# Kernel tuning notes

Hardware: AMD Instinct MI355X
Metric: run time of the kernel (lower is better)

## Reference

```python
import jax, jax.numpy as jnp
from jax import lax
import numpy as np

WAY = 100
SHOT = 5
QUERY = 15
D = 4096
LAM = 10.0
ALPHA = 0.2
N_EPOCHS = 20
EPS = 1e-6
MAXITERS = 1000
N_L = WAY * SHOT          # 500 labeled
N_U = WAY * QUERY         # 1500 unlabeled
N_TOT = N_L + N_U         # 2000


def setup_inputs() -> dict:
    key = jax.random.key(0)
    kx, = jax.random.split(key, 1)
    X = jax.random.uniform(kx, (N_TOT, D), dtype=jnp.float32)  # features must be >= 0
    # data is ordered as (shot+query) blocks of `way` samples, one per class
    labels = jnp.tile(jnp.arange(WAY, dtype=jnp.int32), SHOT + QUERY)
    return {"X": X, "labels": labels}


def _normalize(X):
    # F.normalize(p=2, dim=-1) with eps=1e-12
    return X / jnp.maximum(jnp.linalg.norm(X, axis=-1, keepdims=True), 1e-12)


def _cdist(X, Y):
    # Euclidean distances [n, m] via gram trick (avoids [n, m, d] intermediate)
    d2 = (X * X).sum(-1)[:, None] + (Y * Y).sum(-1)[None, :] - 2.0 * (X @ Y.T)
    return jnp.sqrt(jnp.maximum(d2, 1e-12))


def _sinkhorn(M, r, c):
    # Row/col scaling loop of compute_optimal_transport, tracked via scaling
    # vectors (a, b) so P_k = a * K * b exactly matches the in-place updates.
    K = jnp.exp(-LAM * M)
    K = K / K.sum()
    n, m = M.shape

    def step(carry, _):
        a, b, prev, done = carry
        rowsum = a * (K @ b)                       # P.sum(-1)
        err = jnp.max(jnp.abs(prev - rowsum))      # convergence check vs old u
        done = done | (err <= EPS)
        a_new = jnp.where(done, a, a * r / rowsum)
        colsum = b * (K.T @ a_new)                 # P.sum(1) after row scaling
        b_new = jnp.where(done, b, b * c / colsum)
        prev_new = jnp.where(done, prev, rowsum)
        return (a_new, b_new, prev_new, done), None

    init = (jnp.ones(n, M.dtype), jnp.ones(m, M.dtype),
            jnp.zeros(n, M.dtype), jnp.array(False))
    (a, b, _, _), _ = lax.scan(step, init, None, length=MAXITERS)
    return a[:, None] * K * b[None, :]


def _forward(X, labels):
    # power transform
    X = jnp.sqrt(X + 1e-6)
    # scale (mode='val'): normalize -> center labeled/unlabeled separately -> normalize
    X = _normalize(X)
    Xl = X[:N_L] - X[:N_L].mean(0, keepdims=True)
    Xu = X[N_L:] - X[N_L:].mean(0, keepdims=True)
    Z = _normalize(jnp.concatenate([Xl, Xu], axis=0))

    # init class means from labeled shots
    mus0 = Z.reshape(SHOT + QUERY, WAY, -1)[:SHOT].mean(0)  # [way, d]

    r = jnp.ones(N_U, Z.dtype)
    c = jnp.full((WAY,), float(QUERY), Z.dtype)
    onehot = jax.nn.one_hot(labels[:N_L], WAY, dtype=Z.dtype)

    def get_probas(mus):
        dist = _cdist(Z, mus)                      # [n_tot, way]
        Pu = _sinkhorn(dist[N_L:], r, c)           # [n_u, way]
        return jnp.concatenate([onehot, Pu], axis=0)

    def epoch(mus, _):
        p = get_probas(mus)
        emus = (p.T @ Z) / p.sum(0)[:, None]       # estimate_from_mask
        return mus + ALPHA * (emus - mus), None    # update_from_estimate

    mus, _ = lax.scan(epoch, mus0, None, length=N_EPOCHS)

    P = get_probas(mus)
    logP = jnp.log(P[N_L:] + 1e-5)
    acc = (jnp.argmax(P[N_L:], axis=-1) == labels[N_L:]).astype(jnp.float32).mean()
    return logP, acc


def reference(X, labels):
    return _forward(X, labels)
```

## Files before the change

### kernel.cpp

```cpp
#include <hip/hip_runtime.h>

#define WAY   100
#define SHOT  5
#define NQ    15
#define DD    4096
#define N_L   500
#define N_U   1500
#define N_TOT 2000
#define LAMF  10.0f
#define EPSF  1e-6f
#define MAXIT 1000

#define OFF_Z      0u
#define OFF_CPP    3145728u
#define OFF_MEANL  8192000u
#define OFF_MEANU  8196096u
#define OFF_SL     8200192u
#define OFF_MUSA   8609792u
#define OFF_MUSB   9068544u
#define OFF_MUSQP  9527296u
#define OFF_MUSB16 9552896u
#define OFF_PTH    9782272u
#define OFF_PTL    9868288u
#define OFF_KMAT   9954304u
#define OFF_COLS   10104320u
#define OFF_MISC   10113920u
#define OFF_ZUT    10114688u
#define OFF_ZUTL   13260416u
#define OFF_AG     16406144u
#define OFF_PREVG  16407680u
#define OFF_BINIT  16409216u

#define SINK_BLOCKS 32
#define RPB 47
#define PTS 1536
#define CPS 409600u

typedef __attribute__((ext_vector_type(8))) short short8_t;
typedef __attribute__((ext_vector_type(4))) float f32x4;

__device__ __forceinline__ short f2bs(float f) {
  unsigned u = __float_as_uint(f);
  unsigned r = (u + 0x7FFFu + ((u >> 16) & 1u)) >> 16;
  return (short)r;
}
__device__ __forceinline__ float bs2f(short s) {
  return __uint_as_float(((unsigned)(unsigned short)s) << 16);
}

__global__ __launch_bounds__(256) void k_pow_norm(const float* __restrict__ X, float* __restrict__ Z,
                                                  float* __restrict__ msums, unsigned* __restrict__ misc_u,
                                                  float* __restrict__ aG) {
  int i = blockIdx.x, tid = threadIdx.x;
  __shared__ float red[256];
  if (i < 32) msums[i * 256 + tid] = 0.f;
  if (i == 32) { misc_u[tid] = 0u; misc_u[tid + 256] = 0u; misc_u[tid + 512] = 0u; }
  if (i == 33) { for (int z = tid; z < 1504; z += 256) aG[z] = -1.f; }
  const float* x = X + (size_t)i * DD;
  float s = 0.f;
  for (int k = tid; k < DD; k += 256) s += x[k] + 1e-6f;
  red[tid] = s; __syncthreads();
  for (int o = 128; o > 0; o >>= 1) { if (tid < o) red[tid] += red[tid + o]; __syncthreads(); }
  float inv = 1.0f / fmaxf(sqrtf(red[0]), 1e-12f);
  float* z = Z + (size_t)i * DD;
  for (int k = tid; k < DD; k += 256) z[k] = sqrtf(x[k] + 1e-6f) * inv;
}

__global__ __launch_bounds__(256) void k_colmeans(const float* __restrict__ Z, float* __restrict__ mLs,
                                                  float* __restrict__ mUs) {
  int k = blockIdx.x * 256 + threadIdx.x;
  int r0 = blockIdx.y * 80;
  float sL = 0.f, sU = 0.f;
  for (int r = r0; r < r0 + 80; ++r) {
    float v = Z[(size_t)r * DD + k];
    if (r < N_L) sL += v; else sU += v;
  }
  if (r0 < N_L) atomicAdd(&mLs[k], sL);
  if (r0 + 80 > N_L) atomicAdd(&mUs[k], sU);
}

__global__ __launch_bounds__(256) void k_center(float* __restrict__ Z, const float* __restrict__ mLs,
                                                const float* __restrict__ mUs) {
  int i = blockIdx.x, tid = threadIdx.x;
  __shared__ float red[256];
  const float* m = (i < N_L) ? mLs : mUs;
  const float scale = (i < N_L) ? (1.0f / 500.0f) : (1.0f / 1500.0f);
  float* z = Z + (size_t)i * DD;
  float s = 0.f;
  for (int k = tid; k < DD; k += 256) { float v = z[k] - m[k] * scale; s += v * v; }
  red[tid] = s; __syncthreads();
  for (int o = 128; o > 0; o >>= 1) { if (tid < o) red[tid] += red[tid + o]; __syncthreads(); }
  float inv = 1.0f / fmaxf(sqrtf(red[0]), 1e-12f);
  for (int k = tid; k < DD; k += 256) z[k] = (z[k] - m[k] * scale) * inv;
}

__global__ __launch_bounds__(256) void k_musinit(const float* __restrict__ Z, float* __restrict__ SL,
                                                 float* __restrict__ mus, short* __restrict__ musb,
                                                 float* __restrict__ musqP, float* __restrict__ binit) {
  int w = blockIdx.x, tid = threadIdx.x;
  __shared__ float red[256];
  if (tid == 0) binit[w] = 1.0f;
  float q = 0.f;
  for (int k = tid; k < DD; k += 256) {
    float s = 0.f;
    for (int sh = 0; sh < SHOT; ++sh) s += Z[(size_t)(sh * WAY + w) * DD + k];
    SL[(size_t)w * DD + k] = s;
    float m = s / 5.0f;
    mus[(size_t)w * DD + k] = m;
    musb[(size_t)w * DD + k] = f2bs(m);
    q += m * m;
  }
  red[tid] = q; __syncthreads();
  for (int o = 128; o > 0; o >>= 1) { if (tid < o) red[tid] += red[tid + o]; __syncthreads(); }
  if (tid == 0) musqP[(size_t)w * 256] = red[0];
  else musqP[(size_t)w * 256 + tid] = 0.f;
}

__global__ __launch_bounds__(256) void k_zb(const float* __restrict__ Z, short* __restrict__ Zb, int ubase) {
  size_t i0 = (size_t)ubase * DD + ((size_t)blockIdx.x * 256 + threadIdx.x) * 8;
  short8_t v;
  if (i0 < (size_t)N_U * DD) {
    const float* src = Z + (size_t)N_L * DD + i0;
    float4 a = *(const float4*)src;
    float4 b = *(const float4*)(src + 4);
    v[0] = f2bs(a.x); v[1] = f2bs(a.y); v[2] = f2bs(a.z); v[3] = f2bs(a.w);
    v[4] = f2bs(b.x); v[5] = f2bs(b.y); v[6] = f2bs(b.z); v[7] = f2bs(b.w);
  } else {
    v = (short8_t){0, 0, 0, 0, 0, 0, 0, 0};
  }
  *(short8_t*)(Zb + i0) = v;
}

__global__ __launch_bounds__(256) void k_zt(const float* __restrict__ Z, short* __restrict__ ZTH,
                                            short* __restrict__ ZTL) {
  __shared__ float tile[32][33];
  int k0 = blockIdx.x * 32, u0 = blockIdx.y * 32;
  int c = threadIdx.x & 31, r0 = threadIdx.x >> 5;
#pragma unroll
  for (int rr = 0; rr < 4; ++rr) {
    int r = r0 + rr * 8;
    int u = u0 + r;
    tile[r][c] = (u < N_U) ? Z[(size_t)(N_L + u) * DD + k0 + c] : 0.f;
  }
  __syncthreads();
#pragma unroll
  for (int rr = 0; rr < 4; ++rr) {
    int r = r0 + rr * 8;
    float v = tile[c][r];
    short hi = f2bs(v);
    ZTH[(size_t)(k0 + r) * PTS + u0 + c] = hi;
    ZTL[(size_t)(k0 + r) * PTS + u0 + c] = f2bs(v - bs2f(hi));
  }
}

__global__ __launch_bounds__(256) void k_gemm1K(const short* __restrict__ Zb, const short* __restrict__ musb,
                                                const float* __restrict__ musqP, float* __restrict__ Kmat,
                                                unsigned* __restrict__ misc_u) {
  int tid = threadIdx.x;
  __shared__ float redA[4 * 7 * 4 * 64];
  __shared__ float musq2[2][128];
  if (blockIdx.x == 0) {
    for (int z = tid; z < 768; z += 256) misc_u[z] = 0u;
  }
  {
    int w = tid >> 1, half = tid & 1;
    if (w < WAY) {
      const float* mp = musqP + (size_t)w * 256 + half * 128;
      float q = 0.f;
#pragma unroll 4
      for (int bb = 0; bb < 128; bb += 4) {
        float4 v4 = *(const float4*)(mp + bb);
        q += (v4.x + v4.y) + (v4.z + v4.w);
      }
      musq2[half][w] = q;
    }
  }
  int wv = tid >> 6, l = tid & 63;
  int l15 = l & 15, quad = (l >> 4) & 3;
  int u0 = blockIdx.x * 16;
  f32x4 acc[7];
#pragma unroll
  for (int c = 0; c < 7; ++c) acc[c] = (f32x4){0.f, 0.f, 0.f, 0.f};

  const short* bp = Zb + (size_t)(u0 + l15) * DD + wv * 1024 + quad * 8;
  const short* ap = musb + (size_t)l15 * DD + wv * 1024 + quad * 8;
#pragma unroll 2
  for (int kc = 0; kc < 1024; kc += 32) {
    short8_t bf = *(const short8_t*)(bp + kc);
#pragma unroll
    for (int c = 0; c < 7; ++c) {
      short8_t af = *(const short8_t*)(ap + (size_t)c * 16 * DD + kc);
      acc[c] = __builtin_amdgcn_mfma_f32_16x16x32_bf16(af, bf, acc[c], 0, 0, 0);
    }
  }
#pragma unroll
  for (int c = 0; c < 7; ++c)
#pragma unroll
    for (int r = 0; r < 4; ++r)
      redA[((wv * 7 + c) * 4 + r) * 64 + l] = acc[c][r];
  __syncthreads();
  if (wv == 0) {
    int u = u0 + l15;
#pragma unroll
    for (int c = 0; c < 7; ++c)
#pragma unroll
      for (int r = 0; r < 4; ++r) {
        int base = (c * 4 + r) * 64 + l;
        float s = redA[base] + redA[base + 1792] + redA[base + 3584] + redA[base + 5376];
        int w = 16 * c + quad * 4 + r;
        if (w < WAY && u < N_U) {
          float d2 = 1.0f + (musq2[0][w] + musq2[1][w]) - 2.0f * s;
          Kmat[(size_t)u * WAY + w] = expf(-LAMF * sqrtf(fmaxf(d2, 1e-12f)));
        }
      }
  }
}

__device__ __forceinline__ void gbar(unsigned* slots, unsigned t) {
  __syncthreads();
  if (threadIdx.x == 0) {
    __threadfence();
    __hip_atomic_store(slots + (unsigned)blockIdx.x * 16, t, __ATOMIC_RELEASE, __HIP_MEMORY_SCOPE_AGENT);
  }
  if (threadIdx.x < SINK_BLOCKS) {
    while (__hip_atomic_load(slots + threadIdx.x * 16, __ATOMIC_ACQUIRE, __HIP_MEMORY_SCOPE_AGENT) < t)
      __builtin_amdgcn_s_sleep(1);
  }
  __syncthreads();
}

__global__ __launch_bounds__(256) void k_sink(const float* __restrict__ Kg,
                                              short* __restrict__ PTH, short* __restrict__ PTL,
                                              float* __restrict__ colsP, float* __restrict__ aG,
                                              float* __restrict__ prevG, float* __restrict__ binit,
                                              unsigned* __restrict__ misc_u, float* __restrict__ misc_f) {
  __shared__ float Kl[RPB * WAY];
  __shared__ float a[RPB], aold[RPB], prevs[RPB], b[WAY];
  __shared__ float rerr[256];
  __shared__ float c2[2 * WAY];
  __shared__ float red[256];
  __shared__ float eSh;
  unsigned* slots = misc_u + 8;
  float* KsumG = misc_f + 3;
  int tid = threadIdx.x;
  int row0 = blockIdx.x * RPB;
  int nrows = (row0 + RPB <= N_U) ? RPB : (N_U - row0);

  float ks = 0.f;
  for (int idx = tid; idx < nrows * WAY; idx += 256) { float v = Kg[row0 * WAY + idx]; Kl[idx] = v; ks += v; }
  red[tid] = ks; __syncthreads();
  for (int o = 128; o > 0; o >>= 1) { if (tid < o) red[tid] += red[tid + o]; __syncthreads(); }
  if (tid == 0) atomicAdd(KsumG, red[0]);
  if (tid < WAY) b[tid] = binit[tid];
  unsigned bt = 1;
  gbar(slots, bt);
  float S = *KsumG;
  bool warm = (aG[row0] >= 0.f);
  if (tid < RPB) {
    a[tid] = warm ? aG[row0 + tid] : (1.0f / S);
    prevs[tid] = warm ? prevG[row0 + tid] : 0.f;
  }

  bool conv = false;
  for (int t = 0; t < MAXIT; ++t) {
    float* cp = colsP + (t & 1) * 4096;
    __syncthreads();
    if (tid < nrows) {
      const float* kr = &Kl[tid * WAY];
      float r0 = 0.f, r1 = 0.f, r2 = 0.f, r3 = 0.f;
#pragma unroll 4
      for (int j = 0; j < WAY; j += 4) {
        r0 = fmaf(kr[j], b[j], r0);
        r1 = fmaf(kr[j + 1], b[j + 1], r1);
        r2 = fmaf(kr[j + 2], b[j + 2], r2);
        r3 = fmaf(kr[j + 3], b[j + 3], r3);
      }
      float rs = ((r0 + r1) + (r2 + r3)) * a[tid];
      rerr[tid] = fabsf(prevs[tid] - rs);
      aold[tid] = a[tid];
      a[tid] = a[tid] / rs;
      prevs[tid] = rs;
    } else {
      rerr[tid] = 0.f;
    }
    __syncthreads();
    {
      int j = -1, rlo = 0, rhi = 0, slot = 0;
      if (tid < WAY) { j = tid; rlo = 0; rhi = 24; slot = 0; }
      else if (tid >= 128 && tid < 128 + WAY) { j = tid - 128; rlo = 24; rhi = RPB; slot = 1; }
      if (j >= 0) {
        if (rhi > nrows) rhi = nrows;
        float pc = 0.f;
        for (int r = rlo; r < rhi; ++r) pc = fmaf(Kl[r * WAY + j], a[r], pc);
        c2[slot * WAY + j] = pc;
      }
    }
    __syncthreads();
    if (tid < WAY) cp[(unsigned)blockIdx.x * 128 + tid] = c2[tid] + c2[WAY + tid];
    if (tid < 64) {
      float m = fmaxf(fmaxf(rerr[tid], rerr[tid + 64]), fmaxf(rerr[tid + 128], rerr[tid + 192]));
#pragma unroll
      for (int o = 32; o > 0; o >>= 1) m = fmaxf(m, __shfl_down(m, o));
      if (tid == 0) cp[(unsigned)blockIdx.x * 128 + 100] = m;
    }
    ++bt;
    gbar(slots, bt);
    if (tid < 64) {
      float e = (tid < SINK_BLOCKS) ? cp[tid * 128 + 100] : 0.f;
#pragma unroll
      for (int o = 32; o > 0; o >>= 1) e = fmaxf(e, __shfl_down(e, o));
      if (tid == 0) eSh = e;
    }
    __syncthreads();
    if (eSh <= EPSF) { conv = true; break; }
    if (tid < WAY) {
      float s = 0.f;
#pragma unroll 8
      for (int sb = 0; sb < SINK_BLOCKS; ++sb) s += cp[sb * 128 + tid];
      b[tid] = (float)NQ / s;
    }
  }
  __syncthreads();
  if (tid < nrows) {
    float af = conv ? aold[tid] : a[tid];
    aG[row0 + tid] = af;
    prevG[row0 + tid] = prevs[tid];
  }
  if (blockIdx.x == 0 && tid < WAY) binit[tid] = b[tid];
  for (int idx = tid; idx < WAY * nrows; idx += 256) {
    int j = idx / nrows; int r = idx - j * nrows;
    float av = conv ? aold[r] : a[r];
    float p = av * Kl[r * WAY + j] * b[j];
    short hi = f2bs(p);
    PTH[(size_t)j * PTS + row0 + r] = hi;
    PTL[(size_t)j * PTS + row0 + r] = f2bs(p - bs2f(hi));
  }
  if (blockIdx.x == SINK_BLOCKS - 1) {
    for (int idx = tid; idx < WAY * 4; idx += 256) {
      int j = idx >> 2;
      PTH[(size_t)j * PTS + 1500 + (idx & 3)] = 0;
      PTL[(size_t)j * PTS + 1500 + (idx & 3)] = 0;
    }
  }
}

__global__ __launch_bounds__(64) void k_gemm2(const short* __restrict__ PTH, const short* __restrict__ PTL,
                                              const short* __restrict__ ZTH, const short* __restrict__ ZTL,
                                              float* __restrict__ CPp) {
  int l = threadIdx.x, l15 = l & 15, quad = l >> 4;
  int k0 = blockIdx.x * 16;
  int us = blockIdx.y;
  int kcb = us * 192;
  int kce = (us == 7) ? 1504 : kcb + 192;
  f32x4 acc[7];
#pragma unroll
  for (int c = 0; c < 7; ++c) acc[c] = (f32x4){0.f, 0.f, 0.f, 0.f};
  size_t aoff = (size_t)l15 * PTS + quad * 8;
  const short* bph = ZTH + (size_t)(k0 + l15) * PTS + quad * 8;
  const short* bpl = ZTL + (size_t)(k0 + l15) * PTS + quad * 8;
  for (int kc = kcb; kc < kce; kc += 32) {
    short8_t bh = *(const short8_t*)(bph + kc);
    short8_t bl = *(const short8_t*)(bpl + kc);
#pragma unroll
    for (int c = 0; c < 7; ++c) {
      short8_t ah = *(const short8_t*)(PTH + aoff + (size_t)c * 16 * PTS + kc);
      short8_t al = *(const short8_t*)(PTL + aoff + (size_t)c * 16 * PTS + kc);
      acc[c] = __builtin_amdgcn_mfma_f32_16x16x32_bf16(ah, bh, acc[c], 0, 0, 0);
      acc[c] = __builtin_amdgcn_mfma_f32_16x16x32_bf16(al, bh, acc[c], 0, 0, 0);
      acc[c] = __builtin_amdgcn_mfma_f32_16x16x32_bf16(ah, bl, acc[c], 0, 0, 0);
    }
  }
  float* dst = CPp + (size_t)us * CPS;
#pragma unroll
  for (int c = 0; c < 7; ++c)
#pragma unroll
    for (int r = 0; r < 4; ++r) {
      int w = 16 * c + quad * 4 + r;
      if (w < WAY) dst[(size_t)w * DD + k0 + l15] = acc[c][r];
    }
}

__global__ __launch_bounds__(256) void k_musup(const float* __restrict__ musR, const float* __restrict__ SL,
                                               const float* __restrict__ CPp, float* __restrict__ musW,
                                               short* __restrict__ musb, float* __restrict__ musqP) {
  int w = blockIdx.x, tid = threadIdx.x;
  int kb = blockIdx.y * 1024;
  __shared__ float red[256];
  float q = 0.f;
  for (int k = kb + tid; k < kb + 1024; k += 256) {
    size_t o = (size_t)w * DD + k;
    float c = 0.f;
#pragma unroll
    for (int s = 0; s < 8; ++s) c += CPp[(size_t)s * CPS + o];
    float emus = (SL[o] + c) / 20.0f;
    float m = musR[o];
    float v = m + 0.2f * (emus - m);
    musW[o] = v;
    musb[o] = f2bs(v);
    q += v * v;
  }
  red[tid] = q; __syncthreads();
  for (int o = 128; o > 0; o >>= 1) { if (tid < o) red[tid] += red[tid + o]; __syncthreads(); }
  if (tid == 0) musqP[(size_t)w * 256 + blockIdx.y] = red[0];
}

__global__ __launch_bounds__(128) void k_final(const short* __restrict__ PTH, const short* __restrict__ PTL,
                                               const int* __restrict__ labels, float* __restrict__ out,
                                               unsigned* __restrict__ ctr) {
  int u = blockIdx.x, tid = threadIdx.x;
  __shared__ float vals[WAY];
  if (tid < WAY) {
    float v = bs2f(PTH[(size_t)tid * PTS + u]) + bs2f(PTL[(size_t)tid * PTS + u]);
    vals[tid] = v;
    out[(size_t)u * WAY + tid] = logf(v + 1e-5f);
  }
  __syncthreads();
  if (tid == 0) {
    int am = 0; float bv = vals[0];
    for (int j = 1; j < WAY; ++j) { if (vals[j] > bv) { bv = vals[j]; am = j; } }
    if (am == labels[N_L + u]) atomicAdd(ctr, 1u);
  }
}

__global__ void k_acc(const unsigned* __restrict__ ctr, float* __restrict__ out) {
  if (threadIdx.x == 0) out[N_U * WAY] = (float)(*ctr) / 1500.0f;
}

extern "C" void kernel_launch(void* const* d_in, const int* in_sizes, int n_in,
                              void* d_out, int out_size, void* d_ws, size_t ws_size,
                              hipStream_t stream) {
  const float* X = (const float*)d_in[0];
  const int* labels = (const int*)d_in[1];
  float* out = (float*)d_out;
  float* ws = (float*)d_ws;

  float* Z     = ws + OFF_Z;
  short* Zb    = (short*)(ws + OFF_Z);
  float* CPp   = ws + OFF_CPP;
  float* meanL = ws + OFF_MEANL;
  float* meanU = ws + OFF_MEANU;
  float* SL    = ws + OFF_SL;
  float* musA  = ws + OFF_MUSA;
  float* musB  = ws + OFF_MUSB;
  float* musqP = ws + OFF_MUSQP;
  short* musb16 = (short*)(ws + OFF_MUSB16);
  short* PTH   = (short*)(ws + OFF_PTH);
  short* PTL   = (short*)(ws + OFF_PTL);
  float* Kmat  = ws + OFF_KMAT;
  float* colsP = ws + OFF_COLS;
  float* misc_f = ws + OFF_MISC;
  unsigned* misc_u = (unsigned*)(ws + OFF_MISC);
  short* ZTH   = (short*)(ws + OFF_ZUT);
  short* ZTL   = (short*)(ws + OFF_ZUTL);
  float* aG    = ws + OFF_AG;
  float* prevG = ws + OFF_PREVG;
  float* binit = ws + OFF_BINIT;

  k_pow_norm<<<N_TOT, 256, 0, stream>>>(X, Z, meanL, misc_u, aG);
  k_colmeans<<<dim3(16, 25), 256, 0, stream>>>(Z, meanL, meanU);
  k_center<<<N_TOT, 256, 0, stream>>>(Z, meanL, meanU);
  k_musinit<<<WAY, 256, 0, stream>>>(Z, SL, musA, musb16, musqP, binit);
  k_zt<<<dim3(128, 48), 256, 0, stream>>>(Z, ZTH, ZTL);
  k_zb<<<1536, 256, 0, stream>>>(Z, Zb, 0);
  k_zb<<<1536, 256, 0, stream>>>(Z, Zb, 768);

  float* musR = musA;
  float* musW = musB;
  for (int e = 0; e < 20; ++e) {
    k_gemm1K<<<96, 256, 0, stream>>>(Zb, musb16, musqP, Kmat, misc_u);
    k_sink<<<SINK_BLOCKS, 256, 0, stream>>>(Kmat, PTH, PTL, colsP, aG, prevG, binit, misc_u, misc_f);
    k_gemm2<<<dim3(256, 8), 64, 0, stream>>>(PTH, PTL, ZTH, ZTL, CPp);
    k_musup<<<dim3(WAY, 4), 256, 0, stream>>>(musR, SL, CPp, musW, musb16, musqP);
    float* tmp = musR; musR = musW; musW = tmp;
  }
  k_gemm1K<<<96, 256, 0, stream>>>(Zb, musb16, musqP, Kmat, misc_u);
  k_sink<<<SINK_BLOCKS, 256, 0, stream>>>(Kmat, PTH, PTL, colsP, aG, prevG, binit, misc_u, misc_f);
  k_final<<<N_U, 128, 0, stream>>>(PTH, PTL, labels, out, misc_u + 5);
  k_acc<<<1, 64, 0, stream>>>(misc_u + 5, out);
}
```

Baseline: 2.274 ms.

## Shrink Sinkhorn grid to 8 wide blocks and lighten grid barrier

The persistent Sinkhorn kernel now runs on 8 blocks of 512 threads with 188 rows each, instead of 32 blocks of 256. This cuts the number of participants in the per-iteration grid barrier and the size of the cross-block column reduction. The barrier drops release/acquire fences in favour of an explicit s_waitcnt plus relaxed agent-scope atomics, and the initial barrier is skipped on warm-started epochs. Shared K rows are padded to 101 floats to avoid bank conflicts, and the b update is computed before the convergence sync. In exchange, each block does more serial per-iteration work, and the memory ordering is weaker than before.

```diff
diff --git a/kernel.cpp b/kernel.cpp
--- a/kernel.cpp
+++ b/kernel.cpp
@@ -31,8 +31,10 @@
 #define OFF_PREVG  16407680u
 #define OFF_BINIT  16409216u
 
-#define SINK_BLOCKS 32
-#define RPB 47
+#define SINK_BLOCKS 8
+#define SINK_T 512
+#define RPB 188
+#define KLS 101
 #define PTS 1536
 #define CPS 409600u
 
@@ -46,6 +48,13 @@
 }
 __device__ __forceinline__ float bs2f(short s) {
   return __uint_as_float(((unsigned)(unsigned short)s) << 16);
+}
+
+__device__ __forceinline__ float ld_agent(const float* p) {
+  return __hip_atomic_load(p, __ATOMIC_RELAXED, __HIP_MEMORY_SCOPE_AGENT);
+}
+__device__ __forceinline__ void st_agent(float* p, float v) {
+  __hip_atomic_store(p, v, __ATOMIC_RELAXED, __HIP_MEMORY_SCOPE_AGENT);
 }
 
 __global__ __launch_bounds__(256) void k_pow_norm(const float* __restrict__ X, float* __restrict__ Z,
@@ -219,26 +228,26 @@
 __device__ __forceinline__ void gbar(unsigned* slots, unsigned t) {
   __syncthreads();
   if (threadIdx.x == 0) {
-    __threadfence();
-    __hip_atomic_store(slots + (unsigned)blockIdx.x * 16, t, __ATOMIC_RELEASE, __HIP_MEMORY_SCOPE_AGENT);
+    asm volatile("s_waitcnt vmcnt(0) lgkmcnt(0)" ::: "memory");
+    __hip_atomic_store(slots + (unsigned)blockIdx.x * 16, t, __ATOMIC_RELAXED, __HIP_MEMORY_SCOPE_AGENT);
   }
   if (threadIdx.x < SINK_BLOCKS) {
-    while (__hip_atomic_load(slots + threadIdx.x * 16, __ATOMIC_ACQUIRE, __HIP_MEMORY_SCOPE_AGENT) < t)
+    while (__hip_atomic_load(slots + threadIdx.x * 16, __ATOMIC_RELAXED, __HIP_MEMORY_SCOPE_AGENT) < t)
       __builtin_amdgcn_s_sleep(1);
   }
   __syncthreads();
 }
 
-__global__ __launch_bounds__(256) void k_sink(const float* __restrict__ Kg,
-                                              short* __restrict__ PTH, short* __restrict__ PTL,
-                                              float* __restrict__ colsP, float* __restrict__ aG,
-                                              float* __restrict__ prevG, float* __restrict__ binit,
-                                              unsigned* __restrict__ misc_u, float* __restrict__ misc_f) {
-  __shared__ float Kl[RPB * WAY];
+__global__ __launch_bounds__(SINK_T) void k_sink(const float* __restrict__ Kg,
+                                                 short* __restrict__ PTH, short* __restrict__ PTL,
+                                                 float* __restrict__ colsP, float* __restrict__ aG,
+                                                 float* __restrict__ prevG, float* __restrict__ binit,
+                                                 unsigned* __restrict__ misc_u, float* __restrict__ misc_f) {
+  __shared__ float Kl[RPB * KLS];
   __shared__ float a[RPB], aold[RPB], prevs[RPB], b[WAY];
-  __shared__ float rerr[256];
-  __shared__ float c2[2 * WAY];
-  __shared__ float red[256];
+  __shared__ float rerr[SINK_T];
+  __shared__ float c2[5 * WAY];
+  __shared__ float red[SINK_T];
   __shared__ float eSh;
   unsigned* slots = misc_u + 8;
   float* KsumG = misc_f + 3;
@@ -247,15 +256,21 @@
   int nrows = (row0 + RPB <= N_U) ? RPB : (N_U - row0);
 
   float ks = 0.f;
-  for (int idx = tid; idx < nrows * WAY; idx += 256) { float v = Kg[row0 * WAY + idx]; Kl[idx] = v; ks += v; }
+  for (int idx = tid; idx < nrows * WAY; idx += SINK_T) {
+    float v = Kg[row0 * WAY + idx];
+    int r = idx / WAY, j = idx - r * WAY;
+    Kl[r * KLS + j] = v;
+    ks += v;
+  }
   red[tid] = ks; __syncthreads();
-  for (int o = 128; o > 0; o >>= 1) { if (tid < o) red[tid] += red[tid + o]; __syncthreads(); }
+  for (int o = SINK_T / 2; o > 0; o >>= 1) { if (tid < o) red[tid] += red[tid + o]; __syncthreads(); }
   if (tid == 0) atomicAdd(KsumG, red[0]);
   if (tid < WAY) b[tid] = binit[tid];
-  unsigned bt = 1;
-  gbar(slots, bt);
-  float S = *KsumG;
+
   bool warm = (aG[row0] >= 0.f);
+  unsigned bt = 0;
+  if (!warm) { ++bt; gbar(slots, bt); }
+  float S = warm ? 1.f : ld_agent(KsumG);
   if (tid < RPB) {
     a[tid] = warm ? aG[row0 + tid] : (1.0f / S);
     prevs[tid] = warm ? prevG[row0 + tid] : 0.f;
@@ -266,7 +281,7 @@
     float* cp = colsP + (t & 1) * 4096;
     __syncthreads();
     if (tid < nrows) {
-      const float* kr = &Kl[tid * WAY];
+      const float* kr = &Kl[tid * KLS];
       float r0 = 0.f, r1 = 0.f, r2 = 0.f, r3 = 0.f;
 #pragma unroll 4
       for (int j = 0; j < WAY; j += 4) {
@@ -284,41 +299,47 @@
       rerr[tid] = 0.f;
     }
     __syncthreads();
-    {
-      int j = -1, rlo = 0, rhi = 0, slot = 0;
-      if (tid < WAY) { j = tid; rlo = 0; rhi = 24; slot = 0; }
-      else if (tid >= 128 && tid < 128 + WAY) { j = tid - 128; rlo = 24; rhi = RPB; slot = 1; }
-      if (j >= 0) {
-        if (rhi > nrows) rhi = nrows;
-        float pc = 0.f;
-        for (int r = rlo; r < rhi; ++r) pc = fmaf(Kl[r * WAY + j], a[r], pc);
-        c2[slot * WAY + j] = pc;
-      }
+    if (tid < 500) {
+      int slot = tid / 100;
+      int j = tid - slot * 100;
+      int rlo = slot * 38;
+      int rhi = rlo + 38; if (rhi > nrows) rhi = nrows;
+      float pc = 0.f;
+      for (int r = rlo; r < rhi; ++r) pc = fmaf(Kl[r * KLS + j], a[r], pc);
+      c2[slot * WAY + j] = pc;
     }
     __syncthreads();
-    if (tid < WAY) cp[(unsigned)blockIdx.x * 128 + tid] = c2[tid] + c2[WAY + tid];
+    if (tid < WAY) {
+      float s0 = c2[tid] + c2[WAY + tid] + c2[2 * WAY + tid] + c2[3 * WAY + tid] + c2[4 * WAY + tid];
+      st_agent(cp + (unsigned)blockIdx.x * 128 + tid, s0);
+    }
     if (tid < 64) {
-      float m = fmaxf(fmaxf(rerr[tid], rerr[tid + 64]), fmaxf(rerr[tid + 128], rerr[tid + 192]));
+      float m = rerr[tid];
+#pragma unroll
+      for (int k = 1; k < 8; ++k) m = fmaxf(m, rerr[tid + 64 * k]);
 #pragma unroll
       for (int o = 32; o > 0; o >>= 1) m = fmaxf(m, __shfl_down(m, o));
-      if (tid == 0) cp[(unsigned)blockIdx.x * 128 + 100] = m;
+      if (tid == 0) st_agent(cp + (unsigned)blockIdx.x * 128 + 100, m);
     }
     ++bt;
     gbar(slots, bt);
+    float bnew = 0.f;
+    if (tid >= 256 && tid < 256 + WAY) {
+      int j = tid - 256;
+      float s = 0.f;
+#pragma unroll
+      for (int sb = 0; sb < SINK_BLOCKS; ++sb) s += ld_agent(cp + sb * 128 + j);
+      bnew = (float)NQ / s;
+    }
     if (tid < 64) {
-      float e = (tid < SINK_BLOCKS) ? cp[tid * 128 + 100] : 0.f;
-#pragma unroll
-      for (int o = 32; o > 0; o >>= 1) e = fmaxf(e, __shfl_down(e, o));
+      float e = (tid < SINK_BLOCKS) ? ld_agent(cp + tid * 128 + 100) : 0.f;
+#pragma unroll
+      for (int o = 4; o > 0; o >>= 1) e = fmaxf(e, __shfl_down(e, o));
       if (tid == 0) eSh = e;
     }
     __syncthreads();
     if (eSh <= EPSF) { conv = true; break; }
-    if (tid < WAY) {
-      float s = 0.f;
-#pragma unroll 8
-      for (int sb = 0; sb < SINK_BLOCKS; ++sb) s += cp[sb * 128 + tid];
-      b[tid] = (float)NQ / s;
-    }
+    if (tid >= 256 && tid < 256 + WAY) b[tid - 256] = bnew;
   }
   __syncthreads();
   if (tid < nrows) {
@@ -327,16 +348,16 @@
     prevG[row0 + tid] = prevs[tid];
   }
   if (blockIdx.x == 0 && tid < WAY) binit[tid] = b[tid];
-  for (int idx = tid; idx < WAY * nrows; idx += 256) {
+  for (int idx = tid; idx < WAY * nrows; idx += SINK_T) {
     int j = idx / nrows; int r = idx - j * nrows;
     float av = conv ? aold[r] : a[r];
-    float p = av * Kl[r * WAY + j] * b[j];
+    float p = av * Kl[r * KLS + j] * b[j];
     short hi = f2bs(p);
     PTH[(size_t)j * PTS + row0 + r] = hi;
     PTL[(size_t)j * PTS + row0 + r] = f2bs(p - bs2f(hi));
   }
   if (blockIdx.x == SINK_BLOCKS - 1) {
-    for (int idx = tid; idx < WAY * 4; idx += 256) {
+    for (int idx = tid; idx < WAY * 4; idx += SINK_T) {
       int j = idx >> 2;
       PTH[(size_t)j * PTS + 1500 + (idx & 3)] = 0;
       PTL[(size_t)j * PTS + 1500 + (idx & 3)] = 0;
@@ -468,13 +489,13 @@
   float* musW = musB;
   for (int e = 0; e < 20; ++e) {
     k_gemm1K<<<96, 256, 0, stream>>>(Zb, musb16, musqP, Kmat, misc_u);
-    k_sink<<<SINK_BLOCKS, 256, 0, stream>>>(Kmat, PTH, PTL, colsP, aG, prevG, binit, misc_u, misc_f);
+    k_sink<<<SINK_BLOCKS, SINK_T, 0, stream>>>(Kmat, PTH, PTL, colsP, aG, prevG, binit, misc_u, misc_f);
     k_gemm2<<<dim3(256, 8), 64, 0, stream>>>(PTH, PTL, ZTH, ZTL, CPp);
     k_musup<<<dim3(WAY, 4), 256, 0, stream>>>(musR, SL, CPp, musW, musb16, musqP);
     float* tmp = musR; musR = musW; musW = tmp;
   }
   k_gemm1K<<<96, 256, 0, stream>>>(Zb, musb16, musqP, Kmat, misc_u);
-  k_sink<<<SINK_BLOCKS, 256, 0, stream>>>(Kmat, PTH, PTL, colsP, aG, prevG, binit, misc_u, misc_f);
+  k_sink<<<SINK_BLOCKS, SINK_T, 0, stream>>>(Kmat, PTH, PTL, colsP, aG, prevG, binit, misc_u, misc_f);
   k_final<<<N_U, 128, 0, stream>>>(PTH, PTL, labels, out, misc_u + 5);
   k_acc<<<1, 64, 0, stream>>>(misc_u + 5, out);
 }
```

Result: no change. 2.313 ms (+1.7%).
